# Kernel optimization log

Hardware: AMD Instinct MI355X
Metric: run time of the kernel (lower is better)

## Reference

```python
import jax, jax.numpy as jnp
import numpy as np

N = 20000; DX = 512; DW = 64; DY = 256; M = 320000
DS = DX // 2; DD = DX // 4; DP = DS + DD  # 256, 128, 384
EPS = 1e-9; LN_EPS = 1e-5; SLOPE = 0.05
PNAMES = ['rW1','rb1','rg1','rbt1','rW2','rb2','yW1','yb1','yg1','ybt1','yW2','yb2',
          'iaW1','iab1','iag1','iabt1','iaW2','iab2','cW1','cb1','cg1','cbt1','cW2','cb2']

def _mlp2(h, W1, b1, g, be, W2, b2):
    # Linear -> LayerNorm -> LeakyReLU(0.05) -> Linear  (matches mlp(..., norm='layer'))
    h = h @ W1 + b1
    mu = jnp.mean(h, axis=-1, keepdims=True)
    var = jnp.mean((h - mu) ** 2, axis=-1, keepdims=True)
    h = (h - mu) * jax.lax.rsqrt(var + LN_EPS) * g + be
    h = jnp.where(h >= 0, h, SLOPE * h)
    return h @ W2 + b2

def _m(Pp, n, h):
    return _mlp2(h, Pp[n+'W1'], Pp[n+'b1'], Pp[n+'g1'], Pp[n+'bt1'], Pp[n+'W2'], Pp[n+'b2'])

def _agg(a, b):
    s = a + b
    return jnp.where(s >= 0, s, SLOPE * s)

def _run(x, ei, edge_attr, u_r, u_ia, u_pick, Pp, dec=None):
    """GuoUnpool forward (steps 1a, 2a, 2b). ei: concrete numpy [2,M] int64.
    dec holds concrete sampled decisions; built from the uniforms when None."""
    build = dec is None
    if build:
        dec = {}
    # coalesce (edges are duplicate-free) + lexsort by (src, dst)
    perm = np.argsort(ei[0].astype(np.int64) * N + ei[1].astype(np.int64), kind='stable')
    src, dst = ei[0][perm], ei[1][perm]
    ea = edge_attr[perm]
    # --- step 1a: bernoulli unpool decision per node (I_s = I_u = empty, I_r = all nodes)
    pr = jax.nn.sigmoid(_m(Pp, 'r', x)[:, 0])
    if build:
        dec['choose'] = np.asarray(u_r) < np.asarray(pr)
    choose = dec['choose']
    Iu = np.flatnonzero(choose); Is = np.flatnonzero(~choose)
    logP = jnp.sum(jnp.where(jnp.asarray(choose), jnp.log(pr + EPS), jnp.log(1.0 - pr + EPS)))
    prs = jnp.clip(pr, EPS, 1.0 - EPS)
    ent = -jnp.sum(prs * jnp.log(prs) + (1.0 - prs) * jnp.log(1.0 - prs))
    # --- projections (_ps1_idx = [0:ds+D], _ps2_idx = [0:ds] + [ds+D:ds+2D]) and child embeddings
    ps1 = x[:, :DP]
    ps2 = jnp.concatenate([x[:, :DS], x[:, DS + DD:DS + 2 * DD]], axis=-1)
    y1 = _m(Pp, 'y', ps1)   # [N, dy]; rows at Is give x_static, rows at Iu give x_c1
    y2 = _m(Pp, 'y', ps2)   # rows at Iu give x_c2
    x_out = jnp.concatenate([y1[Is], y1[Iu], y2[Iu]], axis=0)
    # --- step 2a: intra-edge decision for unpooled nodes
    p_ia = jax.nn.sigmoid(_m(Pp, 'ia', _agg(y1[Iu], y2[Iu]))[:, 0])
    if build:
        dec['vc'] = np.asarray(u_ia)[Iu] < np.asarray(p_ia)
    vc = dec['vc']
    logP = logP + jnp.sum(jnp.where(jnp.asarray(vc), jnp.log(p_ia + EPS), jnp.log(1.0 - p_ia + EPS)))
    ps = jnp.clip(p_ia, EPS, 1.0 - EPS)
    ent = ent - jnp.sum(ps * jnp.log(ps) + (1.0 - ps) * jnp.log(1.0 - ps))
    # --- step 2b: categorical neighbor pick for unpooled nodes without intra edge
    if build:
        iun = Iu[~vc]
        par = np.concatenate([src, dst]); nb = np.concatenate([dst, src])
        ek = np.concatenate([np.arange(len(src)), np.arange(len(src))])
        keep = np.zeros(N, dtype=bool); keep[iun] = True
        msk = keep[par]
        par, nb, ek = par[msk], nb[msk], ek[msk]
        o = np.lexsort((nb, par))  # adj lists sorted by neighbor id, grouped by parent
        par, nb, ek = par[o], nb[o], ek[o]
        new = np.r_[True, par[1:] != par[:-1]]
        dec['par'], dec['nb'], dec['ek'] = par, nb, ek
        dec['seg'] = np.cumsum(new) - 1
        dec['starts'] = np.flatnonzero(new)
    par, nb, ek = dec['par'], dec['nb'], dec['ek']
    segn, starts = dec['seg'], dec['starts']
    Pn = len(par); nseg = int(segn[-1]) + 1
    seg = jnp.asarray(segn)
    yagg = _agg(y1, y2)
    feats = jnp.concatenate([yagg[par], ea[ek], x[nb]], axis=-1)  # [Pn, dy+dw+dx]
    scores = _m(Pp, 'c', feats)[:, 0]
    mx = jax.ops.segment_max(scores, seg, num_segments=nseg)
    e = jnp.exp(scores - mx[segn])
    den = jax.ops.segment_sum(e, seg, num_segments=nseg)
    probs = e / den[segn]                      # per-parent softmax over neighbors
    if build:
        # multinomial pick via inverse CDF on the provided per-parent uniform
        p_np = np.asarray(probs).astype(np.float64)
        cum = np.cumsum(p_np)
        base = np.concatenate([[0.0], cum])[starts]
        cumw = cum - base[segn]
        useg = np.asarray(u_pick)[par[starts]][segn]
        cand = np.where(cumw > useg, np.arange(Pn), Pn)
        pick = np.minimum.reduceat(cand, starts)
        last = np.r_[starts[1:] - 1, Pn - 1]
        dec['pick'] = np.minimum(pick, last)
    pick = dec['pick']
    logP = logP + jnp.sum(jnp.log(jnp.clip(probs[pick], EPS, None)))
    pc = jnp.clip(probs, EPS, None)
    ent = ent - jnp.sum(pc * jnp.log(pc))
    return (x_out, logP, ent), dec

def _init_params(key):
    Pp = {}
    specs = [('r', DX, max(1, DX // 2), 1), ('y', DP, 128, DY), ('ia', DY, 128, 1), ('c', DY + DW + DX, 128, 1)]
    ks = jax.random.split(key, len(specs))
    for (n, a, h, o), k in zip(specs, ks):
        k1, k2 = jax.random.split(k)
        Pp[n+'W1'] = jax.random.normal(k1, (a, h), jnp.float32) / np.sqrt(a)
        Pp[n+'b1'] = jnp.zeros((h,), jnp.float32)
        Pp[n+'g1'] = jnp.ones((h,), jnp.float32)
        Pp[n+'bt1'] = jnp.zeros((h,), jnp.float32)
        Pp[n+'W2'] = jax.random.normal(k2, (h, o), jnp.float32) / np.sqrt(h)
        Pp[n+'b2'] = jnp.zeros((o,), jnp.float32)
    return Pp

def setup_inputs() -> dict:
    key = jax.random.key(0)
    k = jax.random.split(key, 6)
    x = jax.random.normal(k[0], (N, DX), jnp.float32)
    rng = np.random.default_rng(0)
    ns = int(M * 1.5)
    s = rng.integers(0, N, ns); d = rng.integers(0, N, ns)
    ok = s != d; s, d = s[ok], d[ok]
    _, ui = np.unique(s.astype(np.int64) * N + d, return_index=True)  # duplicate-free (coalesced)
    sel = rng.permutation(ui)[:M]
    edge_index = jnp.asarray(np.stack([s[sel], d[sel]]).astype(np.int64))
    inp = {
        'x': x,
        'edge_index': edge_index,
        'edge_attr': 0.5 * jax.random.normal(k[1], (M, DW), jnp.float32),
        'u_r': jax.random.uniform(k[2], (N,), jnp.float32),
        'u_ia': jax.random.uniform(k[3], (N,), jnp.float32),
        'u_pick': jax.random.uniform(k[4], (N,), jnp.float32),
    }
    inp.update(_init_params(k[5]))
    return inp

def reference(x, edge_index, edge_attr, u_r, u_ia, u_pick,
              rW1, rb1, rg1, rbt1, rW2, rb2,
              yW1, yb1, yg1, ybt1, yW2, yb2,
              iaW1, iab1, iag1, iabt1, iaW2, iab2,
              cW1, cb1, cg1, cbt1, cW2, cb2):
    Pp = dict(zip(PNAMES, (rW1, rb1, rg1, rbt1, rW2, rb2, yW1, yb1, yg1, ybt1, yW2, yb2,
                           iaW1, iab1, iag1, iabt1, iaW2, iab2, cW1, cb1, cg1, cbt1, cW2, cb2)))
    out, _ = _run(x, np.asarray(edge_index), edge_attr, u_r, u_ia, u_pick, Pp)
    return out
```

## Files before the change

### kernel.cpp

```cpp
#include <hip/hip_runtime.h>
#include <math.h>

#define KN 20000
#define KM 320000

typedef __attribute__((ext_vector_type(8))) short bf16x8;
typedef __attribute__((ext_vector_type(4))) float f32x4;

__device__ __forceinline__ ushort f2bf(float f){
  union{float f; unsigned u;} a; a.f=f;
  unsigned r = a.u + 0x7FFFu + ((a.u>>16)&1u);
  return (ushort)(r>>16);
}
__device__ __forceinline__ float bf2f(ushort u){
  union{unsigned u; float f;} a; a.u=((unsigned)u)<<16; return a.f;
}

__device__ __forceinline__ void blk_add2(double lp, double en, double* acc, double* sh){
#pragma unroll
  for (int o=32;o;o>>=1){ lp+=__shfl_xor(lp,o,64); en+=__shfl_xor(en,o,64); }
  int w=threadIdx.x>>6;
  if ((threadIdx.x&63)==0){ sh[2*w]=lp; sh[2*w+1]=en; }
  __syncthreads();
  if (threadIdx.x==0){
    double L=0,E=0; int nw=(blockDim.x+63)>>6;
    for (int i=0;i<nw;i++){L+=sh[2*i];E+=sh[2*i+1];}
    atomicAdd(&acc[0],L); atomicAdd(&acc[1],E);
  }
  __syncthreads();
}

__global__ void k_init(int* __restrict__ deg,int* __restrict__ fill,int* __restrict__ keep,
                       int* __restrict__ counters,double* __restrict__ acc){
  int i=blockIdx.x*blockDim.x+threadIdx.x;
  if (i<KN){ deg[i]=0; fill[i]=0; keep[i]=0; }
  if (i<8) counters[i]=0;
  if (i<2) acc[i]=0.0;
}

__global__ __launch_bounds__(256) void k_cvt(const float* __restrict__ src, ushort* __restrict__ dst, int n8){
  int i=blockIdx.x*256+threadIdx.x;
  if (i<n8){
    const float* s=src+(size_t)i*8;
    float4 a=*(const float4*)s, b=*(const float4*)(s+4);
    union{ushort u[8]; uint4 v;} o;
    o.u[0]=f2bf(a.x);o.u[1]=f2bf(a.y);o.u[2]=f2bf(a.z);o.u[3]=f2bf(a.w);
    o.u[4]=f2bf(b.x);o.u[5]=f2bf(b.y);o.u[6]=f2bf(b.z);o.u[7]=f2bf(b.w);
    *(uint4*)(dst+(size_t)i*8)=o.v;
  }
}

__global__ __launch_bounds__(256) void k_cvt2(const float* __restrict__ src,
    ushort* __restrict__ hi, ushort* __restrict__ lo, int n8){
  int i=blockIdx.x*256+threadIdx.x;
  if (i<n8){
    const float* s=src+(size_t)i*8;
    union{ushort u[8]; uint4 v;} oh, ol;
#pragma unroll
    for (int j=0;j<8;j++){
      float v=s[j];
      ushort h=f2bf(v);
      oh.u[j]=h;
      ol.u[j]=f2bf(v-bf2f(h));
    }
    *(uint4*)(hi+(size_t)i*8)=oh.v;
    *(uint4*)(lo+(size_t)i*8)=ol.v;
  }
}

__global__ __launch_bounds__(256) void k_prep_w1d(const float* __restrict__ W1, double* __restrict__ w1d){
  int i=blockIdx.x*256+threadIdx.x;
  if (i<512*256) w1d[i]=(double)W1[i];
}
__global__ __launch_bounds__(256) void k_prep_wr2(const float* __restrict__ W1,
    ushort* __restrict__ Wrt_hi, ushort* __restrict__ Wrt_lo){
  int i=blockIdx.x*256+threadIdx.x;
  if (i<512*256){
    int n=i&255, k=i>>8;
    float wv=W1[(size_t)k*256+n];
    ushort h=f2bf(wv);
    int kt=k>>5, kc=(k>>3)&3, j=k&7;
    size_t dst=(((size_t)kt*1024)+(size_t)kc*256+(size_t)n)*8+j;
    Wrt_hi[dst]=h;
    Wrt_lo[dst]=f2bf(wv-bf2f(h));
  }
}

#define RFLAG_TAU 3e-4f
__global__ __launch_bounds__(512) void k_rmlp_fast2(const float* __restrict__ x,
    const ushort* __restrict__ x_hi,const ushort* __restrict__ x_lo,
    const ushort* __restrict__ Wrt_hi,const ushort* __restrict__ Wrt_lo,
    const double* __restrict__ w1d,
    const float* __restrict__ b1,const float* __restrict__ g1,
    const float* __restrict__ bt1,const float* __restrict__ W2,const float* __restrict__ b2,
    const float* __restrict__ u_r, float* __restrict__ pr, int* __restrict__ choose){
  __shared__ __align__(16) ushort Bl[2][2][8192];
  __shared__ float psum[64][2], pvar[64][2], pdot[64][2];
  __shared__ int flagsh[64];
  __shared__ double dsh[256];
  int t=threadIdx.x;
  int w=t>>6, l=t&63;
  int lr=l&15, lk=l>>4;
  int rg=w>>1, ch=w&1;
  int row0=blockIdx.x*64;
  if (t<64) flagsh[t]=0;
  int q0=t*2, q1=t*2+1;
  f32x4 acc[8];
#pragma unroll
  for (int c=0;c<8;c++) acc[c]=(f32x4){0,0,0,0};
  int rowA=row0+rg*16+lr; if (rowA>=KN) rowA=KN-1;
  const ushort* ah=x_hi+(size_t)rowA*512;
  const ushort* al=x_lo+(size_t)rowA*512;
  bf16x8 nh0=*(const bf16x8*)(Wrt_hi+q0*8);
  bf16x8 nh1=*(const bf16x8*)(Wrt_hi+q1*8);
  bf16x8 nl0=*(const bf16x8*)(Wrt_lo+q0*8);
  bf16x8 nl1=*(const bf16x8*)(Wrt_lo+q1*8);
  *(bf16x8*)&Bl[0][0][q0*8]=nh0; *(bf16x8*)&Bl[0][0][q1*8]=nh1;
  *(bf16x8*)&Bl[0][1][q0*8]=nl0; *(bf16x8*)&Bl[0][1][q1*8]=nl1;
  nh0=*(const bf16x8*)(Wrt_hi+8192+q0*8);
  nh1=*(const bf16x8*)(Wrt_hi+8192+q1*8);
  nl0=*(const bf16x8*)(Wrt_lo+8192+q0*8);
  nl1=*(const bf16x8*)(Wrt_lo+8192+q1*8);
  bf16x8 a_h0=*(const bf16x8*)(ah+0*32+lk*8), a_l0=*(const bf16x8*)(al+0*32+lk*8);
  bf16x8 a_h1=*(const bf16x8*)(ah+1*32+lk*8), a_l1=*(const bf16x8*)(al+1*32+lk*8);
  bf16x8 a_h2=*(const bf16x8*)(ah+2*32+lk*8), a_l2=*(const bf16x8*)(al+2*32+lk*8);
  bf16x8 a_h3=*(const bf16x8*)(ah+3*32+lk*8), a_l3=*(const bf16x8*)(al+3*32+lk*8);
  __syncthreads();
#define RBODY(KT,AH,AL) { \
    const int cur_=(KT)&1, nxt_=cur_^1; \
    if ((KT)<15){ \
      *(bf16x8*)&Bl[nxt_][0][q0*8]=nh0; *(bf16x8*)&Bl[nxt_][0][q1*8]=nh1; \
      *(bf16x8*)&Bl[nxt_][1][q0*8]=nl0; *(bf16x8*)&Bl[nxt_][1][q1*8]=nl1; \
      if ((KT)<14){ \
        size_t so_=(size_t)((KT)+2)*8192; \
        nh0=*(const bf16x8*)(Wrt_hi+so_+q0*8); nh1=*(const bf16x8*)(Wrt_hi+so_+q1*8); \
        nl0=*(const bf16x8*)(Wrt_lo+so_+q0*8); nl1=*(const bf16x8*)(Wrt_lo+so_+q1*8); \
      } \
    } \
    bf16x8 uh_=AH, ul_=AL; \
    if ((KT)<12){ \
      int ko_=((KT)+4)*32+lk*8; \
      AH=*(const bf16x8*)(ah+ko_); \
      AL=*(const bf16x8*)(al+ko_); \
    } \
    _Pragma("unroll") \
    for (int c=0;c<8;c++){ \
      int col_=ch*128+c*16+lr; \
      bf16x8 vh_=*(const bf16x8*)&Bl[cur_][0][((lk<<8)+col_)*8]; \
      bf16x8 vl_=*(const bf16x8*)&Bl[cur_][1][((lk<<8)+col_)*8]; \
      acc[c]=__builtin_amdgcn_mfma_f32_16x16x32_bf16(uh_,vh_,acc[c],0,0,0); \
      acc[c]=__builtin_amdgcn_mfma_f32_16x16x32_bf16(uh_,vl_,acc[c],0,0,0); \
      acc[c]=__builtin_amdgcn_mfma_f32_16x16x32_bf16(ul_,vh_,acc[c],0,0,0); \
    } \
    __syncthreads(); \
  }
  RBODY(0,a_h0,a_l0)  RBODY(1,a_h1,a_l1)  RBODY(2,a_h2,a_l2)  RBODY(3,a_h3,a_l3)
  RBODY(4,a_h0,a_l0)  RBODY(5,a_h1,a_l1)  RBODY(6,a_h2,a_l2)  RBODY(7,a_h3,a_l3)
  RBODY(8,a_h0,a_l0)  RBODY(9,a_h1,a_l1)  RBODY(10,a_h2,a_l2) RBODY(11,a_h3,a_l3)
  RBODY(12,a_h0,a_l0) RBODY(13,a_h1,a_l1) RBODY(14,a_h2,a_l2) RBODY(15,a_h3,a_l3)
#undef RBODY
  float b1v[8],g1v[8],btv[8],w2v[8];
#pragma unroll
  for (int c=0;c<8;c++){
    int col=ch*128+c*16+lr;
    b1v[c]=b1[col]; g1v[c]=g1[col]; btv[c]=bt1[col]; w2v[c]=W2[col];
  }
  float hv[4][8];
#pragma unroll
  for (int i=0;i<4;i++){
    float s=0.f;
#pragma unroll
    for (int c=0;c<8;c++){ hv[i][c]=acc[c][i]+b1v[c]; s+=hv[i][c]; }
#pragma unroll
    for (int o=8;o;o>>=1) s+=__shfl_xor(s,o,64);
    if (lr==0) psum[rg*16+lk*4+i][ch]=s;
  }
  __syncthreads();
  float mu_[4];
#pragma unroll
  for (int i=0;i<4;i++){
    int r=rg*16+lk*4+i;
    mu_[i]=(psum[r][0]+psum[r][1])*(1.0f/256.0f);
    float v=0.f;
#pragma unroll
    for (int c=0;c<8;c++){ float d=hv[i][c]-mu_[i]; v+=d*d; }
#pragma unroll
    for (int o=8;o;o>>=1) v+=__shfl_xor(v,o,64);
    if (lr==0) pvar[r][ch]=v;
  }
  __syncthreads();
#pragma unroll
  for (int i=0;i<4;i++){
    int r=rg*16+lk*4+i;
    float rs=1.0f/sqrtf((pvar[r][0]+pvar[r][1])*(1.0f/256.0f)+1e-5f);
    float dot=0.f;
#pragma unroll
    for (int c=0;c<8;c++){
      float hn=(hv[i][c]-mu_[i])*rs*g1v[c]+btv[c];
      hn=hn>=0.f?hn:0.05f*hn;
      dot=fmaf(hn,w2v[c],dot);
    }
#pragma unroll
    for (int o=8;o;o>>=1) dot+=__shfl_xor(dot,o,64);
    if (lr==0) pdot[r][ch]=dot;
  }
  __syncthreads();
  if (t<64){
    int n=row0+t;
    if (n<KN){
      float o2=pdot[t][0]+pdot[t][1]+b2[0];
      float pf=1.0f/(1.0f+expf(-o2));
      float u=u_r[n];
      pr[n]=pf;
      choose[n]=(u<pf)?1:0;
      if (fabsf(pf-u)<RFLAG_TAU) flagsh[t]=1;
    }
  }
  __syncthreads();
  for (int r=0;r<64;r++){
    if (!flagsh[r]) continue;
    int n=row0+r;
    if (t<256){
      double ha=(double)b1[t];
      const float* xr=x+(size_t)n*512;
      for (int k=0;k<512;k++) ha=fma((double)xr[k],w1d[(size_t)k*256+t],ha);
      dsh[t]=ha;
    }
    __syncthreads();
    if (t<64){
      double s=0;
      for (int j=t;j<256;j+=64) s+=dsh[j];
#pragma unroll
      for (int o=32;o;o>>=1) s+=__shfl_xor(s,o,64);
      double mu=s*(1.0/256.0);
      double v=0;
      for (int j=t;j<256;j+=64){ double d=dsh[j]-mu; v+=d*d; }
#pragma unroll
      for (int o=32;o;o>>=1) v+=__shfl_xor(v,o,64);
      double rs=1.0/sqrt(v*(1.0/256.0)+1e-5);
      double dot=0;
      for (int j=t;j<256;j+=64){
        double hn=(dsh[j]-mu)*rs*(double)g1[j]+(double)bt1[j];
        hn = hn>=0.0? hn : 0.05*hn;
        dot=fma(hn,(double)W2[j],dot);
      }
#pragma unroll
      for (int o=32;o;o>>=1) dot+=__shfl_xor(dot,o,64);
      if (t==0){
        double p=1.0/(1.0+exp(-(dot+(double)b2[0])));
        float pf=(float)p;
        pr[n]=pf;
        choose[n]=(u_r[n]<pf)?1:0;
      }
    }
    __syncthreads();
  }
}

__global__ __launch_bounds__(1024) void k_scan_choose(const int* __restrict__ choose,int* __restrict__ excl,
                                                      int* __restrict__ iu,int* __restrict__ counters){
  __shared__ int part[1024];
  const int CH=(KN+1023)/1024;
  int t=threadIdx.x;
  int base=t*CH;
  int s=0;
  for (int i=0;i<CH;i++){int idx=base+i; if (idx<KN) s+=choose[idx];}
  part[t]=s; __syncthreads();
  for (int o=1;o<1024;o<<=1){ int vv=part[t]; int a=(t>=o)?part[t-o]:0; __syncthreads(); part[t]=vv+a; __syncthreads(); }
  int ex=(t>0)?part[t-1]:0;
  for (int i=0;i<CH;i++){
    int idx=base+i;
    if (idx<KN){ int c=choose[idx]; excl[idx]=ex; if (c) iu[ex]=idx; ex+=c; }
  }
  if (t==1023) counters[2]=part[1023];
}

__global__ void k_prep_w1yt(const float* __restrict__ W1, ushort* __restrict__ W1yt){
  int i=blockIdx.x*256+threadIdx.x;
  if (i<384*128){
    int n=i&127, k=i>>7;
    W1yt[(size_t)n*384+k]=f2bf(W1[(size_t)k*128+n]);
  }
}
__global__ void k_prep_w2yt(const float* __restrict__ W2, ushort* __restrict__ W2yt){
  int i=blockIdx.x*256+threadIdx.x;
  if (i<128*256){
    int n=i&255, k=i>>8;
    W2yt[(size_t)n*128+k]=f2bf(W2[(size_t)k*256+n]);
  }
}

#define YEXTP 261
__global__ __launch_bounds__(256) void k_ymlp_v2(const ushort* __restrict__ x_bf,
    const ushort* __restrict__ W1yt,const float* __restrict__ b1,const float* __restrict__ g1,
    const float* __restrict__ bt1,const ushort* __restrict__ W2yt,const float* __restrict__ b2,
    const int* __restrict__ choose,const int* __restrict__ excl,int cnt,
    float* __restrict__ yagg_f,ushort* __restrict__ yagg_bf,
    float* __restrict__ out){
  __shared__ __align__(16) char smem[16896+8704];
  float*  hf  =(float*)smem;
  float*  yext=(float*)smem;
  ushort* hb  =(ushort*)(smem+16896);
  int t=threadIdx.x;
  int w=t>>6, l=t&63;
  int lr=l&15, lk=l>>4;
  int md=w&1, kh=w>>1;
  int row0=blockIdx.x*16;
  f32x4 acc[8];
#pragma unroll
  for (int c=0;c<8;c++) acc[c]=(f32x4){0,0,0,0};
  const ushort* xr=x_bf+(size_t)(row0+lr)*512;
#pragma unroll
  for (int kt=0;kt<6;kt++){
    int k0=kh*192+kt*32+lk*8;
    int ks=(md && k0>=256)? k0+128 : k0;
    bf16x8 a=*(const bf16x8*)(xr+ks);
#pragma unroll
    for (int c=0;c<8;c++){
      bf16x8 b=*(const bf16x8*)(W1yt+(size_t)(c*16+lr)*384+k0);
      acc[c]=__builtin_amdgcn_mfma_f32_16x16x32_bf16(a,b,acc[c],0,0,0);
    }
  }
  if (kh==0){
#pragma unroll
    for (int i=0;i<4;i++){
      int row=lk*4+i;
#pragma unroll
      for (int c=0;c<8;c++) hf[((size_t)md*16+row)*132+c*16+lr]=acc[c][i];
    }
  }
  __syncthreads();
  if (kh==1){
    float b1v[8],g1v[8],btv[8];
#pragma unroll
    for (int c=0;c<8;c++){ int col=c*16+lr; b1v[c]=b1[col]; g1v[c]=g1[col]; btv[c]=bt1[col]; }
#pragma unroll
    for (int i=0;i<4;i++){
      int row=lk*4+i;
      float hv[8]; float s=0.f;
#pragma unroll
      for (int c=0;c<8;c++){ hv[c]=acc[c][i]+hf[((size_t)md*16+row)*132+c*16+lr]+b1v[c]; s+=hv[c]; }
#pragma unroll
      for (int o=8;o;o>>=1) s+=__shfl_xor(s,o,64);
      float mu=s*(1.0f/128.0f);
      float v=0.f;
#pragma unroll
      for (int c=0;c<8;c++){ float d=hv[c]-mu; v+=d*d; }
#pragma unroll
      for (int o=8;o;o>>=1) v+=__shfl_xor(v,o,64);
      float rs=1.0f/sqrtf(v*(1.0f/128.0f)+1e-5f);
      ushort* hrow=hb+((size_t)md*16+row)*136;
#pragma unroll
      for (int c=0;c<8;c++){
        float hn=(hv[c]-mu)*rs*g1v[c]+btv[c];
        hn=hn>=0.f?hn:0.05f*hn;
        hrow[c*16+lr]=f2bf(hn);
      }
    }
  }
  __syncthreads();
  f32x4 acc2[8];
#pragma unroll
  for (int c=0;c<8;c++) acc2[c]=(f32x4){0,0,0,0};
  const ushort* ha=hb+((size_t)md*16+lr)*136;
#pragma unroll
  for (int kt=0;kt<4;kt++){
    bf16x8 a=*(const bf16x8*)(ha+kt*32+lk*8);
#pragma unroll
    for (int c=0;c<8;c++){
      bf16x8 b=*(const bf16x8*)(W2yt+(size_t)(kh*128+c*16+lr)*128+kt*32+lk*8);
      acc2[c]=__builtin_amdgcn_mfma_f32_16x16x32_bf16(a,b,acc2[c],0,0,0);
    }
  }
  float b2v[8];
#pragma unroll
  for (int c=0;c<8;c++) b2v[c]=b2[kh*128+c*16+lr];
  if (md==0){
#pragma unroll
    for (int i=0;i<4;i++){
      int row=lk*4+i;
#pragma unroll
      for (int c=0;c<8;c++) yext[(size_t)row*YEXTP+kh*128+c*16+lr]=acc2[c][i]+b2v[c];
    }
  }
  __syncthreads();
  if (md==0){
#pragma unroll
    for (int i=0;i<4;i++){
      int row=lk*4+i, n=row0+row;
      int cch=choose[n], ex=excl[n];
      int r1 = cch? (KN-cnt)+ex : n-ex;
      if (r1>=0 && r1<KN+cnt){
        float* orow=out+(size_t)r1*256+kh*128;
#pragma unroll
        for (int c=0;c<8;c++) orow[c*16+lr]=acc2[c][i]+b2v[c];
      }
    }
  } else {
#pragma unroll
    for (int i=0;i<4;i++){
      int row=lk*4+i, n=row0+row;
      int cch=choose[n], ex=excl[n];
      size_t base=(size_t)n*256+kh*128;
#pragma unroll
      for (int c=0;c<8;c++){
        int colk=c*16+lr;
        float v2=acc2[c][i]+b2v[c];
        float v1=yext[(size_t)row*YEXTP+kh*128+colk];
        float ga=v1+v2; ga=ga>=0.f?ga:0.05f*ga;
        yagg_f[base+colk]=ga;
        yagg_bf[base+colk]=f2bf(ga);
        if (cch){ int r2=KN+ex; if (r2<KN+cnt) out[(size_t)r2*256+kh*128+colk]=v2; }
      }
    }
  }
}

__global__ __launch_bounds__(256) void k_node_term(const float* __restrict__ pr,const int* __restrict__ choose,
                                                   double* __restrict__ acc){
  __shared__ double sh[8];
  int i=blockIdx.x*256+threadIdx.x;
  double lp=0,en=0;
  if (i<KN){
    double p=(double)pr[i];
    lp = choose[i]? log(p+1e-9) : log(1.0-p+1e-9);
    double ps=fmin(fmax(p,1e-9),1.0-1e-9);
    en = -(ps*log(ps)+(1.0-ps)*log(1.0-ps));
  }
  blk_add2(lp,en,acc,sh);
}

__global__ __launch_bounds__(128) void k_ia(const float* __restrict__ yagg_f,
    const int* __restrict__ iu,const float* __restrict__ u_ia,
    const float* __restrict__ W1,const float* __restrict__ b1,const float* __restrict__ g1,
    const float* __restrict__ bt1,const float* __restrict__ W2,const float* __restrict__ b2,
    float* __restrict__ p_ia,int* __restrict__ vc,int* __restrict__ keep,double* __restrict__ acc,int cnt){
  __shared__ float insh[8][256];
  __shared__ float hsh[8][128];
  __shared__ double sh[8];
  int t=threadIdx.x;
  int row0=blockIdx.x*8;
  for (int i=t;i<8*256;i+=128){
    int r=i>>8,k=i&255;
    int row=row0+r;
    if (row<cnt){
      unsigned n=(unsigned)iu[row];
      if (n<KN) insh[r][k]=yagg_f[(size_t)n*256+k];
      else insh[r][k]=0.f;
    }
  }
  __syncthreads();
  float accv[8]; float bb=b1[t];
#pragma unroll
  for (int r=0;r<8;r++) accv[r]=bb;
  for (int k=0;k<256;k+=4){
    float w0=W1[(k+0)*128+t],w1=W1[(k+1)*128+t],w2=W1[(k+2)*128+t],w3=W1[(k+3)*128+t];
#pragma unroll
    for (int r=0;r<8;r++){
      float4 f=*(const float4*)&insh[r][k];
      accv[r]=fmaf(f.x,w0,accv[r]); accv[r]=fmaf(f.y,w1,accv[r]); accv[r]=fmaf(f.z,w2,accv[r]); accv[r]=fmaf(f.w,w3,accv[r]);
    }
  }
#pragma unroll
  for (int r=0;r<8;r++) hsh[r][t]=accv[r];
  __syncthreads();
  int g=t>>4, tl=t&15;
  float hv[8];
#pragma unroll
  for (int j=0;j<8;j++) hv[j]=hsh[g][tl+16*j];
  float s=0;
#pragma unroll
  for (int j=0;j<8;j++) s+=hv[j];
#pragma unroll
  for (int o=8;o;o>>=1) s+=__shfl_xor(s,o,64);
  float mu=s*(1.0f/128.0f);
  float v=0;
#pragma unroll
  for (int j=0;j<8;j++){float d=hv[j]-mu; v+=d*d;}
#pragma unroll
  for (int o=8;o;o>>=1) v+=__shfl_xor(v,o,64);
  float rs=1.0f/sqrtf(v*(1.0f/128.0f)+1e-5f);
  float dot=0;
#pragma unroll
  for (int j=0;j<8;j++){
    int idx=tl+16*j;
    float hn=(hv[j]-mu)*rs*g1[idx]+bt1[idx];
    hn=hn>=0.f?hn:0.05f*hn;
    dot=fmaf(hn,W2[idx],dot);
  }
#pragma unroll
  for (int o=8;o;o>>=1) dot+=__shfl_xor(dot,o,64);
  double lp=0,en=0;
  if (tl==0){
    int row=row0+g;
    if (row<cnt){
      unsigned n=(unsigned)iu[row];
      if (n<KN){
        float o=dot+b2[0];
        double p=1.0/(1.0+exp(-(double)o));
        float pf=(float)p;
        p_ia[row]=pf;
        int vv=(u_ia[n]<pf)?1:0;
        vc[row]=vv;
        if(!vv) keep[n]=1;
        lp = vv? log((double)pf+1e-9) : log(1.0-(double)pf+1e-9);
        double ps=fmin(fmax((double)pf,1e-9),1.0-1e-9);
        en = -(ps*log(ps)+(1.0-ps)*log(1.0-ps));
      }
    }
  }
  blk_add2(lp,en,acc,sh);
}

__global__ void k_count(const int* __restrict__ ei,const int* __restrict__ keep,int* __restrict__ deg){
  int e=blockIdx.x*256+threadIdx.x;
  if (e<KM){
    int s=ei[e], d=ei[KM+e];
    if (keep[s]) atomicAdd(&deg[s],1);
    if (keep[d]) atomicAdd(&deg[d],1);
  }
}

__global__ __launch_bounds__(1024) void k_scan_deg(const int* __restrict__ deg,int* __restrict__ boff,
                                                   int* __restrict__ nodeseg,int* __restrict__ counters){
  __shared__ int part[1024];
  const int CH=(KN+1023)/1024;
  int t=threadIdx.x;
  int base=t*CH;
  int s=0;
  for (int i=0;i<CH;i++){int idx=base+i; if(idx<KN) s+=deg[idx];}
  part[t]=s; __syncthreads();
  for (int o=1;o<1024;o<<=1){ int vv=part[t]; int a=(t>=o)?part[t-o]:0; __syncthreads(); part[t]=vv+a; __syncthreads(); }
  int ex=(t>0)?part[t-1]:0;
  for (int i=0;i<CH;i++){int idx=base+i; if(idx<KN){ boff[idx]=ex; ex+=deg[idx]; }}
  if (t==1023){ boff[KN]=part[1023]; counters[0]=part[1023]; }
  __syncthreads();
  s=0;
  for (int i=0;i<CH;i++){int idx=base+i; if(idx<KN) s+=(deg[idx]>0)?1:0;}
  part[t]=s; __syncthreads();
  for (int o=1;o<1024;o<<=1){ int vv=part[t]; int a=(t>=o)?part[t-o]:0; __syncthreads(); part[t]=vv+a; __syncthreads(); }
  ex=(t>0)?part[t-1]:0;
  for (int i=0;i<CH;i++){int idx=base+i; if(idx<KN && deg[idx]>0){ nodeseg[ex]=idx; ex++; }}
  if (t==1023) counters[1]=part[1023];
}

__global__ void k_fill(const int* __restrict__ ei,const int* __restrict__ keep,const int* __restrict__ boff,
                       int* __restrict__ fill,int* __restrict__ parA,int* __restrict__ keyA,int* __restrict__ ekA){
  int e=blockIdx.x*256+threadIdx.x;
  if (e<KM){
    int s=ei[e], d=ei[KM+e];
    if (keep[s]){ int pos=boff[s]+atomicAdd(&fill[s],1); parA[pos]=s; keyA[pos]=d*2;   ekA[pos]=e; }
    if (keep[d]){ int pos=boff[d]+atomicAdd(&fill[d],1); parA[pos]=d; keyA[pos]=s*2+1; ekA[pos]=e; }
  }
}

__global__ void k_rank(const int* __restrict__ parA,const int* __restrict__ keyA,const int* __restrict__ ekA,
                       const int* __restrict__ boff,const int* __restrict__ counters,
                       int* __restrict__ parS,int* __restrict__ nbS,int* __restrict__ ekS){
  int i=blockIdx.x*256+threadIdx.x;
  int Pn=counters[0];
  if (i<Pn){
    int par=parA[i], key=keyA[i];
    int lo=boff[par], hi=boff[par+1];
    int rank=0;
    for (int j=lo;j<hi;j++) rank += (keyA[j]<key)?1:0;
    int pos=lo+rank;
    parS[pos]=par; nbS[pos]=key>>1; ekS[pos]=ekA[i];
  }
}

__global__ void k_prep_w1t(const float* __restrict__ W1, ushort* __restrict__ W1t){
  int i=blockIdx.x*256+threadIdx.x;
  if (i<832*128){
    int n=i&127, k=i>>7;
    W1t[(size_t)n*832+k]=f2bf(W1[(size_t)k*128+n]);
  }
}

__global__ __launch_bounds__(256) void k_hpre_v3(const ushort* __restrict__ yagg_bf,
    const ushort* __restrict__ x_bf,const ushort* __restrict__ W1t,
    float* __restrict__ hyP,float* __restrict__ hxP){
  int t=threadIdx.x;
  int w=t>>6, l=t&63;
  int lr=l&15, lk=l>>4;
  int row0=blockIdx.x*16;
  int cq=w&1;
  f32x4 acc[4];
#pragma unroll
  for (int c=0;c<4;c++) acc[c]=(f32x4){0,0,0,0};
  if (w<2){
    const ushort* ar=yagg_bf+(size_t)(row0+lr)*256+lk*8;
#pragma unroll
    for (int kt=0;kt<8;kt++){
      bf16x8 a=*(const bf16x8*)(ar+kt*32);
#pragma unroll
      for (int c=0;c<4;c++){
        bf16x8 b=*(const bf16x8*)(W1t+(size_t)(cq*64+c*16+lr)*832+kt*32+lk*8);
        acc[c]=__builtin_amdgcn_mfma_f32_16x16x32_bf16(a,b,acc[c],0,0,0);
      }
    }
#pragma unroll
    for (int i=0;i<4;i++){
      int n=row0+lk*4+i;
      float4 v; v.x=acc[0][i]; v.y=acc[1][i]; v.z=acc[2][i]; v.w=acc[3][i];
      *(float4*)(hyP+(size_t)n*128+lr*8+cq*4)=v;
    }
  } else {
    const ushort* ar=x_bf+(size_t)(row0+lr)*512+lk*8;
#pragma unroll
    for (int kt=0;kt<16;kt++){
      bf16x8 a=*(const bf16x8*)(ar+kt*32);
#pragma unroll
      for (int c=0;c<4;c++){
        bf16x8 b=*(const bf16x8*)(W1t+(size_t)(cq*64+c*16+lr)*832+320+kt*32+lk*8);
        acc[c]=__builtin_amdgcn_mfma_f32_16x16x32_bf16(a,b,acc[c],0,0,0);
      }
    }
#pragma unroll
    for (int i=0;i<4;i++){
      int n=row0+lk*4+i;
      float4 v; v.x=acc[0][i]; v.y=acc[1][i]; v.z=acc[2][i]; v.w=acc[3][i];
      *(float4*)(hxP+(size_t)n*128+lr*8+cq*4)=v;
    }
  }
}

__global__ __launch_bounds__(256) void k_cscore_v5(
    const ushort* __restrict__ ea_bf,const float* __restrict__ hyP,const float* __restrict__ hxP,
    const int* __restrict__ parS,const int* __restrict__ nbS,const int* __restrict__ ekS,
    const int* __restrict__ counters,
    const ushort* __restrict__ W1t,const float* __restrict__ b1,const float* __restrict__ g1,
    const float* __restrict__ bt1,const float* __restrict__ W2,const float* __restrict__ b2,
    float* __restrict__ scores){
  int Pn=counters[0];
  if (Pn<=0) return;
  int t=threadIdx.x;
  int w=t>>6, l=t&63;
  int lr=l&15, lk=l>>4;
  float b2s=b2[0];
  float b1v[8],g1v[8],btv[8],w2v[8];
#pragma unroll
  for (int c=0;c<8;c++){
    int col=c*16+lr;
    b1v[c]=b1[col]; g1v[c]=g1[col]; btv[c]=bt1[col]; w2v[c]=W2[col];
  }
  int ngrp=(Pn+63)>>6;
  for (int g=blockIdx.x; g<ngrp; g+=gridDim.x){
    int p0=g*64+w*16;
    float hs[4][8];
#pragma unroll
    for (int i=0;i<4;i++){
      int p=p0+lk*4+i; int pc=p<Pn?p:Pn-1;
      const float* hyp=hyP+(size_t)parS[pc]*128+lr*8;
      const float* hxp=hxP+(size_t)nbS[pc]*128+lr*8;
      float4 ya=*(const float4*)hyp, yb=*(const float4*)(hyp+4);
      float4 xa=*(const float4*)hxp, xb=*(const float4*)(hxp+4);
      hs[i][0]=ya.x+xa.x; hs[i][1]=ya.y+xa.y; hs[i][2]=ya.z+xa.z; hs[i][3]=ya.w+xa.w;
      hs[i][4]=yb.x+xb.x; hs[i][5]=yb.y+xb.y; hs[i][6]=yb.z+xb.z; hs[i][7]=yb.w+xb.w;
    }
    int pA=p0+lr; int ca=pA<Pn?pA:Pn-1;
    const ushort* eaA=ea_bf+(size_t)ekS[ca]*64;
    f32x4 acc[8];
#pragma unroll
    for (int c=0;c<8;c++) acc[c]=(f32x4){0,0,0,0};
#pragma unroll
    for (int kt=0;kt<2;kt++){
      bf16x8 a=*(const bf16x8*)(eaA+kt*32+lk*8);
#pragma unroll
      for (int c=0;c<8;c++){
        bf16x8 b=*(const bf16x8*)(W1t+(size_t)(c*16+lr)*832+256+kt*32+lk*8);
        acc[c]=__builtin_amdgcn_mfma_f32_16x16x32_bf16(a,b,acc[c],0,0,0);
      }
    }
#pragma unroll
    for (int i=0;i<4;i++){
      float hv[8]; float s=0.f;
#pragma unroll
      for (int c=0;c<8;c++){ hv[c]=acc[c][i]+hs[i][c]+b1v[c]; s+=hv[c]; }
#pragma unroll
      for (int o=8;o;o>>=1) s+=__shfl_xor(s,o,64);
      float mu=s*(1.0f/128.0f);
      float v=0.f;
#pragma unroll
      for (int c=0;c<8;c++){ float d=hv[c]-mu; v+=d*d; }
#pragma unroll
      for (int o=8;o;o>>=1) v+=__shfl_xor(v,o,64);
      float rs=1.0f/sqrtf(v*(1.0f/128.0f)+1e-5f);
      float dot=0.f;
#pragma unroll
      for (int c=0;c<8;c++){
        float hn=(hv[c]-mu)*rs*g1v[c]+btv[c];
        hn=hn>=0.f?hn:0.05f*hn;
        dot=fmaf(hn,w2v[c],dot);
      }
#pragma unroll
      for (int o=8;o;o>>=1) dot+=__shfl_xor(dot,o,64);
      if (lr==0){
        int prow=p0+lk*4+i;
        if (prow<Pn) scores[prow]=dot+b2s;
      }
    }
  }
}

__global__ __launch_bounds__(256) void k_segment(const float* __restrict__ scores,const int* __restrict__ boff,
    const int* __restrict__ nodeseg,const int* __restrict__ counters,const float* __restrict__ u_pick,
    double* __restrict__ acc){
  __shared__ double sh[8];
  int nseg=counters[1];
  int s=blockIdx.x*256+threadIdx.x;
  double lp=0,en=0;
  if (s<nseg){
    int n=nodeseg[s];
    int lo=boff[n],hi=boff[n+1];
    float mx=-1e30f;
    for (int p=lo;p<hi;p++) mx=fmaxf(mx,scores[p]);
    float den=0;
    for (int p=lo;p<hi;p++) den+=expf(scores[p]-mx);
    double u=(double)u_pick[n];
    double cum=0; float ppick=-1.f; float plast=0.f;
    for (int p=lo;p<hi;p++){
      float e=expf(scores[p]-mx);
      float prob=e/den;
      double pc=fmax((double)prob,1e-9);
      en -= pc*log(pc);
      plast=prob;
      if (ppick<0.f){ cum+=(double)prob; if (cum>u) ppick=prob; }
    }
    if (ppick<0.f) ppick=plast;
    lp=log(fmax((double)ppick,1e-9));
  }
  blk_add2(lp,en,acc,sh);
}

__global__ void k_final(const double* __restrict__ acc,float* __restrict__ out,int cnt){
  if (threadIdx.x==0 && blockIdx.x==0){
    size_t base=(size_t)(KN+cnt)*256;
    out[base]=(float)acc[0];
    out[base+1]=(float)acc[1];
  }
}

extern "C" void kernel_launch(void* const* d_in,const int* in_sizes,int n_in,
                              void* d_out,int out_size,void* d_ws,size_t ws_size,
                              hipStream_t stream){
  const float* x     =(const float*)d_in[0];
  const int*   ei    =(const int*)  d_in[1];
  const float* ea    =(const float*)d_in[2];
  const float* u_r   =(const float*)d_in[3];
  const float* u_ia  =(const float*)d_in[4];
  const float* u_pick=(const float*)d_in[5];
  const float* Pp[24];
  for (int i=0;i<24;i++) Pp[i]=(const float*)d_in[6+i];
  float* out=(float*)d_out;
  int cnt=(out_size-2)/256 - KN;
  if (cnt<0) cnt=0;

  char* w=(char*)d_ws;
  size_t off=0;
  auto carve=[&](size_t bytes)->char*{ off=(off+255)&~(size_t)255; char* p=w+off; off+=bytes; return p; };
  int*    counters=(int*)   carve(64);
  double* acc     =(double*)carve(64);
  float*  pr      =(float*) carve((size_t)KN*4);
  int*    choose  =(int*)   carve((size_t)KN*4);
  int*    excl    =(int*)   carve((size_t)KN*4);
  int*    iu      =(int*)   carve((size_t)KN*4);
  float*  p_ia    =(float*) carve((size_t)KN*4);
  int*    vc      =(int*)   carve((size_t)KN*4);
  int*    keep    =(int*)   carve((size_t)KN*4);
  int*    deg     =(int*)   carve((size_t)KN*4);
  int*    fill    =(int*)   carve((size_t)KN*4);
  int*    boff    =(int*)   carve((size_t)(KN+1)*4);
  int*    nodeseg =(int*)   carve((size_t)KN*4);
  int*    parA    =(int*)   carve((size_t)2*KM*4);
  int*    keyA    =(int*)   carve((size_t)2*KM*4);
  int*    ekA     =(int*)   carve((size_t)2*KM*4);
  int*    parS    =(int*)   carve((size_t)2*KM*4);
  int*    nbS     =(int*)   carve((size_t)2*KM*4);
  int*    ekS     =(int*)   carve((size_t)2*KM*4);
  float*  scores  =(float*) carve((size_t)2*KM*4);
  float*  yagg_f  =(float*) carve((size_t)KN*256*4);
  ushort* yagg_bf =(ushort*)carve((size_t)KN*256*2);
  ushort* ea_bf   =(ushort*)carve((size_t)KM*64*2);
  ushort* x_bf    =(ushort*)carve((size_t)KN*512*2);
  ushort* x_lo    =(ushort*)carve((size_t)KN*512*2);
  ushort* W1t     =(ushort*)carve((size_t)832*128*2);
  double* w1d     =(double*)carve((size_t)512*256*8);
  ushort* W1yt    =(ushort*)carve((size_t)128*384*2);
  ushort* W2yt    =(ushort*)carve((size_t)256*128*2);
  ushort* Wrt_hi  =(ushort*)carve((size_t)256*512*2);
  ushort* Wrt_lo  =(ushort*)carve((size_t)256*512*2);
  float*  hy      =(float*) carve((size_t)KN*128*4);
  float*  hx      =(float*) carve((size_t)KN*128*4);
  (void)ws_size;(void)n_in;(void)in_sizes;

  k_init<<<(KN+255)/256,256,0,stream>>>(deg,fill,keep,counters,acc);
  k_prep_w1t<<<(832*128+255)/256,256,0,stream>>>(Pp[18],W1t);
  k_prep_w1yt<<<(384*128+255)/256,256,0,stream>>>(Pp[6],W1yt);
  k_prep_w2yt<<<(128*256+255)/256,256,0,stream>>>(Pp[10],W2yt);
  k_prep_wr2<<<(512*256+255)/256,256,0,stream>>>(Pp[0],Wrt_hi,Wrt_lo);
  k_prep_w1d<<<(512*256+255)/256,256,0,stream>>>(Pp[0],w1d);
  k_cvt<<<(KM*64/8+255)/256,256,0,stream>>>(ea,ea_bf,KM*64/8);
  k_cvt2<<<(KN*512/8+255)/256,256,0,stream>>>(x,x_bf,x_lo,KN*512/8);
  k_rmlp_fast2<<<(KN+63)/64,512,0,stream>>>(x,x_bf,x_lo,Wrt_hi,Wrt_lo,w1d,
      Pp[1],Pp[2],Pp[3],Pp[4],Pp[5],u_r,pr,choose);
  k_scan_choose<<<1,1024,0,stream>>>(choose,excl,iu,counters);
  k_ymlp_v2<<<KN/16,256,0,stream>>>(x_bf,W1yt,Pp[7],Pp[8],Pp[9],W2yt,Pp[11],choose,excl,cnt,yagg_f,yagg_bf,out);
  k_hpre_v3<<<KN/16,256,0,stream>>>(yagg_bf,x_bf,W1t,hy,hx);
  k_node_term<<<(KN+255)/256,256,0,stream>>>(pr,choose,acc);
  if (cnt>0)
    k_ia<<<(cnt+7)/8,128,0,stream>>>(yagg_f,iu,u_ia,Pp[12],Pp[13],Pp[14],Pp[15],Pp[16],Pp[17],p_ia,vc,keep,acc,cnt);
  k_count<<<(KM+255)/256,256,0,stream>>>(ei,keep,deg);
  k_scan_deg<<<1,1024,0,stream>>>(deg,boff,nodeseg,counters);
  k_fill<<<(KM+255)/256,256,0,stream>>>(ei,keep,boff,fill,parA,keyA,ekA);
  k_rank<<<(2*KM+255)/256,256,0,stream>>>(parA,keyA,ekA,boff,counters,parS,nbS,ekS);
  k_cscore_v5<<<2560,256,0,stream>>>(ea_bf,hy,hx,parS,nbS,ekS,counters,W1t,Pp[19],Pp[20],Pp[21],Pp[22],Pp[23],scores);
  k_segment<<<(KN+255)/256,256,0,stream>>>(scores,boff,nodeseg,counters,u_pick,acc);
  k_final<<<1,64,0,stream>>>(acc,out,cnt);
}
```

Measured before the change: 494.7 us.

## Drop LDS double-buffering in r-MLP GEMM, read weights directly from global

```diff
diff --git a/kernel.cpp b/kernel.cpp
--- a/kernel.cpp
+++ b/kernel.cpp
@@ -87,78 +87,45 @@
 }
 
 #define RFLAG_TAU 3e-4f
-__global__ __launch_bounds__(512) void k_rmlp_fast2(const float* __restrict__ x,
+__global__ __launch_bounds__(256) void k_rmlp_v3(const float* __restrict__ x,
     const ushort* __restrict__ x_hi,const ushort* __restrict__ x_lo,
     const ushort* __restrict__ Wrt_hi,const ushort* __restrict__ Wrt_lo,
     const double* __restrict__ w1d,
     const float* __restrict__ b1,const float* __restrict__ g1,
     const float* __restrict__ bt1,const float* __restrict__ W2,const float* __restrict__ b2,
     const float* __restrict__ u_r, float* __restrict__ pr, int* __restrict__ choose){
-  __shared__ __align__(16) ushort Bl[2][2][8192];
-  __shared__ float psum[64][2], pvar[64][2], pdot[64][2];
-  __shared__ int flagsh[64];
+  __shared__ float psum[32][2], pvar[32][2], pdot[32][2];
+  __shared__ int flagsh[32];
   __shared__ double dsh[256];
   int t=threadIdx.x;
   int w=t>>6, l=t&63;
   int lr=l&15, lk=l>>4;
   int rg=w>>1, ch=w&1;
-  int row0=blockIdx.x*64;
-  if (t<64) flagsh[t]=0;
-  int q0=t*2, q1=t*2+1;
+  int row0=blockIdx.x*32;
+  if (t<32) flagsh[t]=0;
   f32x4 acc[8];
 #pragma unroll
   for (int c=0;c<8;c++) acc[c]=(f32x4){0,0,0,0};
   int rowA=row0+rg*16+lr; if (rowA>=KN) rowA=KN-1;
   const ushort* ah=x_hi+(size_t)rowA*512;
   const ushort* al=x_lo+(size_t)rowA*512;
-  bf16x8 nh0=*(const bf16x8*)(Wrt_hi+q0*8);
-  bf16x8 nh1=*(const bf16x8*)(Wrt_hi+q1*8);
-  bf16x8 nl0=*(const bf16x8*)(Wrt_lo+q0*8);
-  bf16x8 nl1=*(const bf16x8*)(Wrt_lo+q1*8);
-  *(bf16x8*)&Bl[0][0][q0*8]=nh0; *(bf16x8*)&Bl[0][0][q1*8]=nh1;
-  *(bf16x8*)&Bl[0][1][q0*8]=nl0; *(bf16x8*)&Bl[0][1][q1*8]=nl1;
-  nh0=*(const bf16x8*)(Wrt_hi+8192+q0*8);
-  nh1=*(const bf16x8*)(Wrt_hi+8192+q1*8);
-  nl0=*(const bf16x8*)(Wrt_lo+8192+q0*8);
-  nl1=*(const bf16x8*)(Wrt_lo+8192+q1*8);
-  bf16x8 a_h0=*(const bf16x8*)(ah+0*32+lk*8), a_l0=*(const bf16x8*)(al+0*32+lk*8);
-  bf16x8 a_h1=*(const bf16x8*)(ah+1*32+lk*8), a_l1=*(const bf16x8*)(al+1*32+lk*8);
-  bf16x8 a_h2=*(const bf16x8*)(ah+2*32+lk*8), a_l2=*(const bf16x8*)(al+2*32+lk*8);
-  bf16x8 a_h3=*(const bf16x8*)(ah+3*32+lk*8), a_l3=*(const bf16x8*)(al+3*32+lk*8);
-  __syncthreads();
-#define RBODY(KT,AH,AL) { \
-    const int cur_=(KT)&1, nxt_=cur_^1; \
-    if ((KT)<15){ \
-      *(bf16x8*)&Bl[nxt_][0][q0*8]=nh0; *(bf16x8*)&Bl[nxt_][0][q1*8]=nh1; \
-      *(bf16x8*)&Bl[nxt_][1][q0*8]=nl0; *(bf16x8*)&Bl[nxt_][1][q1*8]=nl1; \
-      if ((KT)<14){ \
-        size_t so_=(size_t)((KT)+2)*8192; \
-        nh0=*(const bf16x8*)(Wrt_hi+so_+q0*8); nh1=*(const bf16x8*)(Wrt_hi+so_+q1*8); \
-        nl0=*(const bf16x8*)(Wrt_lo+so_+q0*8); nl1=*(const bf16x8*)(Wrt_lo+so_+q1*8); \
-      } \
-    } \
-    bf16x8 uh_=AH, ul_=AL; \
-    if ((KT)<12){ \
-      int ko_=((KT)+4)*32+lk*8; \
-      AH=*(const bf16x8*)(ah+ko_); \
-      AL=*(const bf16x8*)(al+ko_); \
-    } \
-    _Pragma("unroll") \
-    for (int c=0;c<8;c++){ \
-      int col_=ch*128+c*16+lr; \
-      bf16x8 vh_=*(const bf16x8*)&Bl[cur_][0][((lk<<8)+col_)*8]; \
-      bf16x8 vl_=*(const bf16x8*)&Bl[cur_][1][((lk<<8)+col_)*8]; \
-      acc[c]=__builtin_amdgcn_mfma_f32_16x16x32_bf16(uh_,vh_,acc[c],0,0,0); \
-      acc[c]=__builtin_amdgcn_mfma_f32_16x16x32_bf16(uh_,vl_,acc[c],0,0,0); \
-      acc[c]=__builtin_amdgcn_mfma_f32_16x16x32_bf16(ul_,vh_,acc[c],0,0,0); \
-    } \
-    __syncthreads(); \
-  }
-  RBODY(0,a_h0,a_l0)  RBODY(1,a_h1,a_l1)  RBODY(2,a_h2,a_l2)  RBODY(3,a_h3,a_l3)
-  RBODY(4,a_h0,a_l0)  RBODY(5,a_h1,a_l1)  RBODY(6,a_h2,a_l2)  RBODY(7,a_h3,a_l3)
-  RBODY(8,a_h0,a_l0)  RBODY(9,a_h1,a_l1)  RBODY(10,a_h2,a_l2) RBODY(11,a_h3,a_l3)
-  RBODY(12,a_h0,a_l0) RBODY(13,a_h1,a_l1) RBODY(14,a_h2,a_l2) RBODY(15,a_h3,a_l3)
-#undef RBODY
+  const ushort* bh0=Wrt_hi+((size_t)lk*256+ch*128)*8;
+  const ushort* bl0=Wrt_lo+((size_t)lk*256+ch*128)*8;
+#pragma unroll 4
+  for (int kt=0;kt<16;kt++){
+    bf16x8 uh=*(const bf16x8*)(ah+kt*32+lk*8);
+    bf16x8 ul=*(const bf16x8*)(al+kt*32+lk*8);
+    const ushort* bh=bh0+(size_t)kt*8192;
+    const ushort* bl=bl0+(size_t)kt*8192;
+#pragma unroll
+    for (int c=0;c<8;c++){
+      bf16x8 vh=*(const bf16x8*)(bh+(c*16+lr)*8);
+      bf16x8 vl=*(const bf16x8*)(bl+(c*16+lr)*8);
+      acc[c]=__builtin_amdgcn_mfma_f32_16x16x32_bf16(uh,vh,acc[c],0,0,0);
+      acc[c]=__builtin_amdgcn_mfma_f32_16x16x32_bf16(uh,vl,acc[c],0,0,0);
+      acc[c]=__builtin_amdgcn_mfma_f32_16x16x32_bf16(ul,vh,acc[c],0,0,0);
+    }
+  }
   float b1v[8],g1v[8],btv[8],w2v[8];
 #pragma unroll
   for (int c=0;c<8;c++){
@@ -205,7 +172,7 @@
     if (lr==0) pdot[r][ch]=dot;
   }
   __syncthreads();
-  if (t<64){
+  if (t<32){
     int n=row0+t;
     if (n<KN){
       float o2=pdot[t][0]+pdot[t][1]+b2[0];
@@ -217,10 +184,10 @@
     }
   }
   __syncthreads();
-  for (int r=0;r<64;r++){
+  for (int r=0;r<32;r++){
     if (!flagsh[r]) continue;
     int n=row0+r;
-    if (t<256){
+    {
       double ha=(double)b1[t];
       const float* xr=x+(size_t)n*512;
       for (int k=0;k<512;k++) ha=fma((double)xr[k],w1d[(size_t)k*256+t],ha);
@@ -802,7 +769,7 @@
   k_prep_w1d<<<(512*256+255)/256,256,0,stream>>>(Pp[0],w1d);
   k_cvt<<<(KM*64/8+255)/256,256,0,stream>>>(ea,ea_bf,KM*64/8);
   k_cvt2<<<(KN*512/8+255)/256,256,0,stream>>>(x,x_bf,x_lo,KN*512/8);
-  k_rmlp_fast2<<<(KN+63)/64,512,0,stream>>>(x,x_bf,x_lo,Wrt_hi,Wrt_lo,w1d,
+  k_rmlp_v3<<<(KN+31)/32,256,0,stream>>>(x,x_bf,x_lo,Wrt_hi,Wrt_lo,w1d,
       Pp[1],Pp[2],Pp[3],Pp[4],Pp[5],u_r,pr,choose);
   k_scan_choose<<<1,1024,0,stream>>>(choose,excl,iu,counters);
   k_ymlp_v2<<<KN/16,256,0,stream>>>(x_bf,W1yt,Pp[7],Pp[8],Pp[9],W2yt,Pp[11],choose,excl,cnt,yagg_f,yagg_bf,out);
```

Result: slower. 506.0 us (+2.3%).

## Fuse edge-attr bf16 conversion into cscore and use wave-shuffle block scans

Applied to the files above, without the earlier changes.

```diff
diff --git a/kernel.cpp b/kernel.cpp
--- a/kernel.cpp
+++ b/kernel.cpp
@@ -36,18 +36,6 @@
   if (i<KN){ deg[i]=0; fill[i]=0; keep[i]=0; }
   if (i<8) counters[i]=0;
   if (i<2) acc[i]=0.0;
-}
-
-__global__ __launch_bounds__(256) void k_cvt(const float* __restrict__ src, ushort* __restrict__ dst, int n8){
-  int i=blockIdx.x*256+threadIdx.x;
-  if (i<n8){
-    const float* s=src+(size_t)i*8;
-    float4 a=*(const float4*)s, b=*(const float4*)(s+4);
-    union{ushort u[8]; uint4 v;} o;
-    o.u[0]=f2bf(a.x);o.u[1]=f2bf(a.y);o.u[2]=f2bf(a.z);o.u[3]=f2bf(a.w);
-    o.u[4]=f2bf(b.x);o.u[5]=f2bf(b.y);o.u[6]=f2bf(b.z);o.u[7]=f2bf(b.w);
-    *(uint4*)(dst+(size_t)i*8)=o.v;
-  }
 }
 
 __global__ __launch_bounds__(256) void k_cvt2(const float* __restrict__ src,
@@ -259,20 +247,23 @@
 
 __global__ __launch_bounds__(1024) void k_scan_choose(const int* __restrict__ choose,int* __restrict__ excl,
                                                       int* __restrict__ iu,int* __restrict__ counters){
-  __shared__ int part[1024];
+  __shared__ int wsum[16], woff[16];
   const int CH=(KN+1023)/1024;
-  int t=threadIdx.x;
+  int t=threadIdx.x, lane=t&63, wid=t>>6;
   int base=t*CH;
   int s=0;
   for (int i=0;i<CH;i++){int idx=base+i; if (idx<KN) s+=choose[idx];}
-  part[t]=s; __syncthreads();
-  for (int o=1;o<1024;o<<=1){ int vv=part[t]; int a=(t>=o)?part[t-o]:0; __syncthreads(); part[t]=vv+a; __syncthreads(); }
-  int ex=(t>0)?part[t-1]:0;
+  int inc=s;
+  for (int o=1;o<64;o<<=1){ int v=__shfl_up(inc,o,64); if (lane>=o) inc+=v; }
+  if (lane==63) wsum[wid]=inc;
+  __syncthreads();
+  if (t==0){ int r=0; for (int i=0;i<16;i++){ woff[i]=r; r+=wsum[i]; } counters[2]=r; }
+  __syncthreads();
+  int ex=woff[wid]+inc-s;
   for (int i=0;i<CH;i++){
     int idx=base+i;
     if (idx<KN){ int c=choose[idx]; excl[idx]=ex; if (c) iu[ex]=idx; ex+=c; }
   }
-  if (t==1023) counters[2]=part[1023];
 }
 
 __global__ void k_prep_w1yt(const float* __restrict__ W1, ushort* __restrict__ W1yt){
@@ -523,25 +514,29 @@
 
 __global__ __launch_bounds__(1024) void k_scan_deg(const int* __restrict__ deg,int* __restrict__ boff,
                                                    int* __restrict__ nodeseg,int* __restrict__ counters){
-  __shared__ int part[1024];
+  __shared__ int wsum[16], woff[16];
   const int CH=(KN+1023)/1024;
-  int t=threadIdx.x;
+  int t=threadIdx.x, lane=t&63, wid=t>>6;
   int base=t*CH;
-  int s=0;
-  for (int i=0;i<CH;i++){int idx=base+i; if(idx<KN) s+=deg[idx];}
-  part[t]=s; __syncthreads();
-  for (int o=1;o<1024;o<<=1){ int vv=part[t]; int a=(t>=o)?part[t-o]:0; __syncthreads(); part[t]=vv+a; __syncthreads(); }
-  int ex=(t>0)?part[t-1]:0;
+  int s=0, sc=0;
+  for (int i=0;i<CH;i++){int idx=base+i; if(idx<KN){ int d=deg[idx]; s+=d; sc+=(d>0)?1:0; }}
+  int inc=s;
+  for (int o=1;o<64;o<<=1){ int v=__shfl_up(inc,o,64); if (lane>=o) inc+=v; }
+  if (lane==63) wsum[wid]=inc;
+  __syncthreads();
+  if (t==0){ int r=0; for (int i=0;i<16;i++){ woff[i]=r; r+=wsum[i]; } boff[KN]=r; counters[0]=r; }
+  __syncthreads();
+  int ex=woff[wid]+inc-s;
   for (int i=0;i<CH;i++){int idx=base+i; if(idx<KN){ boff[idx]=ex; ex+=deg[idx]; }}
-  if (t==1023){ boff[KN]=part[1023]; counters[0]=part[1023]; }
-  __syncthreads();
-  s=0;
-  for (int i=0;i<CH;i++){int idx=base+i; if(idx<KN) s+=(deg[idx]>0)?1:0;}
-  part[t]=s; __syncthreads();
-  for (int o=1;o<1024;o<<=1){ int vv=part[t]; int a=(t>=o)?part[t-o]:0; __syncthreads(); part[t]=vv+a; __syncthreads(); }
-  ex=(t>0)?part[t-1]:0;
-  for (int i=0;i<CH;i++){int idx=base+i; if(idx<KN && deg[idx]>0){ nodeseg[ex]=idx; ex++; }}
-  if (t==1023) counters[1]=part[1023];
+  __syncthreads();
+  int inc2=sc;
+  for (int o=1;o<64;o<<=1){ int v=__shfl_up(inc2,o,64); if (lane>=o) inc2+=v; }
+  if (lane==63) wsum[wid]=inc2;
+  __syncthreads();
+  if (t==0){ int r=0; for (int i=0;i<16;i++){ woff[i]=r; r+=wsum[i]; } counters[1]=r; }
+  __syncthreads();
+  int ex2=woff[wid]+inc2-sc;
+  for (int i=0;i<CH;i++){int idx=base+i; if(idx<KN && deg[idx]>0){ nodeseg[ex2]=idx; ex2++; }}
 }
 
 __global__ void k_fill(const int* __restrict__ ei,const int* __restrict__ keep,const int* __restrict__ boff,
@@ -625,8 +620,8 @@
   }
 }
 
-__global__ __launch_bounds__(256) void k_cscore_v5(
-    const ushort* __restrict__ ea_bf,const float* __restrict__ hyP,const float* __restrict__ hxP,
+__global__ __launch_bounds__(256) void k_cscore_v6(
+    const float* __restrict__ ea,const float* __restrict__ hyP,const float* __restrict__ hxP,
     const int* __restrict__ parS,const int* __restrict__ nbS,const int* __restrict__ ekS,
     const int* __restrict__ counters,
     const ushort* __restrict__ W1t,const float* __restrict__ b1,const float* __restrict__ g1,
@@ -659,13 +654,18 @@
       hs[i][4]=yb.x+xb.x; hs[i][5]=yb.y+xb.y; hs[i][6]=yb.z+xb.z; hs[i][7]=yb.w+xb.w;
     }
     int pA=p0+lr; int ca=pA<Pn?pA:Pn-1;
-    const ushort* eaA=ea_bf+(size_t)ekS[ca]*64;
+    const float* eaA=ea+(size_t)ekS[ca]*64;
     f32x4 acc[8];
 #pragma unroll
     for (int c=0;c<8;c++) acc[c]=(f32x4){0,0,0,0};
 #pragma unroll
     for (int kt=0;kt<2;kt++){
-      bf16x8 a=*(const bf16x8*)(eaA+kt*32+lk*8);
+      float4 fa=*(const float4*)(eaA+kt*32+lk*8);
+      float4 fb=*(const float4*)(eaA+kt*32+lk*8+4);
+      union{ushort u[8]; bf16x8 v;} A;
+      A.u[0]=f2bf(fa.x); A.u[1]=f2bf(fa.y); A.u[2]=f2bf(fa.z); A.u[3]=f2bf(fa.w);
+      A.u[4]=f2bf(fb.x); A.u[5]=f2bf(fb.y); A.u[6]=f2bf(fb.z); A.u[7]=f2bf(fb.w);
+      bf16x8 a=A.v;
 #pragma unroll
       for (int c=0;c<8;c++){
         bf16x8 b=*(const bf16x8*)(W1t+(size_t)(c*16+lr)*832+256+kt*32+lk*8);
@@ -781,7 +781,6 @@
   float*  scores  =(float*) carve((size_t)2*KM*4);
   float*  yagg_f  =(float*) carve((size_t)KN*256*4);
   ushort* yagg_bf =(ushort*)carve((size_t)KN*256*2);
-  ushort* ea_bf   =(ushort*)carve((size_t)KM*64*2);
   ushort* x_bf    =(ushort*)carve((size_t)KN*512*2);
   ushort* x_lo    =(ushort*)carve((size_t)KN*512*2);
   ushort* W1t     =(ushort*)carve((size_t)832*128*2);
@@ -800,7 +799,6 @@
   k_prep_w2yt<<<(128*256+255)/256,256,0,stream>>>(Pp[10],W2yt);
   k_prep_wr2<<<(512*256+255)/256,256,0,stream>>>(Pp[0],Wrt_hi,Wrt_lo);
   k_prep_w1d<<<(512*256+255)/256,256,0,stream>>>(Pp[0],w1d);
-  k_cvt<<<(KM*64/8+255)/256,256,0,stream>>>(ea,ea_bf,KM*64/8);
   k_cvt2<<<(KN*512/8+255)/256,256,0,stream>>>(x,x_bf,x_lo,KN*512/8);
   k_rmlp_fast2<<<(KN+63)/64,512,0,stream>>>(x,x_bf,x_lo,Wrt_hi,Wrt_lo,w1d,
       Pp[1],Pp[2],Pp[3],Pp[4],Pp[5],u_r,pr,choose);
@@ -814,7 +812,7 @@
   k_scan_deg<<<1,1024,0,stream>>>(deg,boff,nodeseg,counters);
   k_fill<<<(KM+255)/256,256,0,stream>>>(ei,keep,boff,fill,parA,keyA,ekA);
   k_rank<<<(2*KM+255)/256,256,0,stream>>>(parA,keyA,ekA,boff,counters,parS,nbS,ekS);
-  k_cscore_v5<<<2560,256,0,stream>>>(ea_bf,hy,hx,parS,nbS,ekS,counters,W1t,Pp[19],Pp[20],Pp[21],Pp[22],Pp[23],scores);
+  k_cscore_v6<<<2560,256,0,stream>>>(ea,hy,hx,parS,nbS,ekS,counters,W1t,Pp[19],Pp[20],Pp[21],Pp[22],Pp[23],scores);
   k_segment<<<(KN+255)/256,256,0,stream>>>(scores,boff,nodeseg,counters,u_pick,acc);
   k_final<<<1,64,0,stream>>>(acc,out,cnt);
 }
```

New measurement: 460.8 us. 1.07x faster.
